# Optimization experiments

Measured on AMD Instinct MI355X. Metric: run time of the kernel, lower is better.

## Reference

```python
import jax, jax.numpy as jnp
import numpy as np

PERIODS = (1, 2, 4, 8)
B, T, D_IN, D_OUT = 64, 2048, 256, 512
N = D_OUT // len(PERIODS)  # 128, per-clock-group width


def setup_inputs() -> dict:
    key = jax.random.key(0)
    ks = jax.random.split(key, 5)
    scale = 1.0 / np.sqrt(N)  # glorot-ish for the (n,n) recurrent mats
    return {
        "X": jax.random.normal(ks[0], (B, T, D_IN), jnp.float32),
        "W": jax.random.uniform(ks[1], (D_IN, D_OUT), jnp.float32, -0.05, 0.05),
        "b": jnp.zeros((D_OUT,), jnp.float32),
        "W_gate": jax.random.uniform(ks[2], (D_IN, D_OUT), jnp.float32, -0.05, 0.05),
        "b_gate": jnp.zeros((D_OUT,), jnp.float32),
        "clock_u": jax.random.normal(ks[3], (len(PERIODS), N, N), jnp.float32) * scale,
        "clock_gates": jax.random.normal(ks[4], (len(PERIODS), N, N), jnp.float32) * scale,
    }


def _hard_sigmoid(x):
    # keras/theano hard_sigmoid: clip(0.2*x + 0.5, 0, 1)
    return jnp.clip(0.2 * x + 0.5, 0.0, 1.0)


def _gating(x_sub, u, u_gate):
    # Faithful to the source: clock_gating passes x_t[:, slice] for ALL THREE of
    # x_t_sub, x_gate_sub, h_tm1_sub (a bug in the original, preserved here).
    k = x_sub @ u                                  # [B, n]
    z = _hard_sigmoid(x_sub + k)                   # update gate (inner_activation)
    q = (x_sub * x_sub) @ u_gate                   # p = x_gate*h_tm1 -> x_sub*x_sub
    z_gate = jnp.tanh(q)                           # gate_activation
    z_out = jax.nn.softplus(x_sub * z_gate)        # activation(s), s = h_tm1*z_gate
    return z * z_out + (1.0 - z) * x_sub           # h_tm1 := x_sub per source bug


def reference(X, W, b, W_gate, b_gate, clock_u, clock_gates):
    # X: [B,T,D_in] -> time-major projections [T,B,D_out]
    x_t = jnp.einsum("bti,io->tbo", X, W) + b
    # x_gate is computed in the source but never consumed due to the slicing
    # bug in clock_gating; DCE'd under jit.
    x_gate = jnp.einsum("bti,io->tbo", X, W_gate) + b_gate  # noqa: F841

    def step(h, inp):
        t, xt = inp
        parts = []
        for i, p in enumerate(PERIODS):
            x_sub = xt[:, i * N:(i + 1) * N]
            new = _gating(x_sub, clock_u[i], clock_gates[i])
            parts.append(jnp.where(t % p == 0, new, h[:, i * N:(i + 1) * N]))
        return jnp.concatenate(parts, axis=1), None

    h0 = jnp.zeros((X.shape[0], D_OUT), X.dtype)
    hT, _ = jax.lax.scan(step, h0, (jnp.arange(x_t.shape[0]), x_t))
    return hT  # return_sequences=False -> last hidden state, [B, D_out]
```

## Files before the change

### kernel.cpp

```cpp
#include <hip/hip_runtime.h>
#include <math.h>


#define TT    2048
#define DIN   256
#define DOUT  512
#define NSUB  128
#define BDIM  64
#define ROWS  8

__global__ __launch_bounds__(256)
void cgrnn_collapsed_kernel(const float* __restrict__ X,
                            const float* __restrict__ W,
                            const float* __restrict__ bias,
                            const float* __restrict__ clock_u,
                            const float* __restrict__ clock_g,
                            float* __restrict__ out)
{
    const int g   = blockIdx.x & 3;
    const int rb  = blockIdx.x >> 2;
    const int r0  = rb * ROWS;
    const int tid = threadIdx.x;
    const int c4  = tid & 31;
    const int r   = tid >> 5;
    const int c   = c4 * 4;

    const int p  = 1 << g;
    const int t  = 2047 - (2047 & (p - 1));

    __shared__ float Xs[ROWS][DIN];
    __shared__ float xs[ROWS][NSUB + 4];

    {
        for (int idx = tid; idx < ROWS * (DIN / 4); idx += 256) {
            const int rr = idx >> 6;
            const int ii = idx & 63;
            const float4 v = *reinterpret_cast<const float4*>(
                X + ((size_t)(r0 + rr) * TT + t) * DIN + ii * 4);
            *reinterpret_cast<float4*>(&Xs[rr][ii * 4]) = v;
        }
    }
    __syncthreads();

    float a0, a1, a2, a3;
    {
        const float* bb = bias + g * NSUB + c;
        a0 = bb[0]; a1 = bb[1]; a2 = bb[2]; a3 = bb[3];
        const float* Wc = W + g * NSUB + c;
#pragma unroll 16
        for (int k = 0; k < DIN; ++k) {
            const float xk = Xs[r][k];
            const float4 wv = *reinterpret_cast<const float4*>(Wc + (size_t)k * DOUT);
            a0 = fmaf(xk, wv.x, a0);
            a1 = fmaf(xk, wv.y, a1);
            a2 = fmaf(xk, wv.z, a2);
            a3 = fmaf(xk, wv.w, a3);
        }
        xs[r][c + 0] = a0;
        xs[r][c + 1] = a1;
        xs[r][c + 2] = a2;
        xs[r][c + 3] = a3;
    }
    __syncthreads();

    float k0 = 0.f, k1 = 0.f, k2 = 0.f, k3 = 0.f;
    float q0 = 0.f, q1 = 0.f, q2 = 0.f, q3 = 0.f;
    {
        const float* ub = clock_u + (size_t)g * NSUB * NSUB + c;
        const float* gb = clock_g + (size_t)g * NSUB * NSUB + c;
#pragma unroll 8
        for (int j = 0; j < NSUB; ++j) {
            const float xv  = xs[r][j];
            const float xv2 = xv * xv;
            const float4 uv = *reinterpret_cast<const float4*>(ub + j * NSUB);
            const float4 gv = *reinterpret_cast<const float4*>(gb + j * NSUB);
            k0 = fmaf(xv, uv.x, k0);  k1 = fmaf(xv, uv.y, k1);
            k2 = fmaf(xv, uv.z, k2);  k3 = fmaf(xv, uv.w, k3);
            q0 = fmaf(xv2, gv.x, q0); q1 = fmaf(xv2, gv.y, q1);
            q2 = fmaf(xv2, gv.z, q2); q3 = fmaf(xv2, gv.w, q3);
        }
    }

    float xr[4] = {a0, a1, a2, a3};
    float kk[4] = {k0, k1, k2, k3};
    float qq[4] = {q0, q1, q2, q3};
    float4 res;
    float* rp = reinterpret_cast<float*>(&res);
#pragma unroll
    for (int i = 0; i < 4; ++i) {
        const float x  = xr[i];
        float z = 0.2f * (x + kk[i]) + 0.5f;
        z = fminf(fmaxf(z, 0.0f), 1.0f);
        const float zg = tanhf(qq[i]);
        const float a  = x * zg;
        const float zo = fmaxf(a, 0.0f) + log1pf(expf(-fabsf(a)));
        rp[i] = z * zo + (1.0f - z) * x;
    }

    *reinterpret_cast<float4*>(out + (size_t)(r0 + r) * DOUT + g * NSUB + c) = res;
}

extern "C" void kernel_launch(void* const* d_in, const int* in_sizes, int n_in,
                              void* d_out, int out_size, void* d_ws, size_t ws_size,
                              hipStream_t stream)
{
    const float* X       = (const float*)d_in[0];
    const float* W       = (const float*)d_in[1];
    const float* bias    = (const float*)d_in[2];
    const float* clock_u = (const float*)d_in[5];
    const float* clock_g = (const float*)d_in[6];
    float* out           = (float*)d_out;

    dim3 grid(4 * (BDIM / ROWS));
    dim3 block(256);
    cgrnn_collapsed_kernel<<<grid, block, 0, stream>>>(X, W, bias, clock_u, clock_g, out);
}
```

Measured before the change: 199.9 us.

## Split reduction across warps and launch one block per batch row and group

Each block now handles one batch row for one clock group instead of eight rows. The input-projection and recurrent-matrix dot products are split across the eight warps along the reduction dimension, then combined through shared-memory partial sums. This raises the grid from 32 to 256 blocks and shortens each thread's serial FMA chain, to fill more compute units and cut latency. In exchange, weights are fetched once per batch row rather than shared across eight rows, and the kernel adds extra barriers and shared-memory traffic.

```diff
diff --git a/kernel.cpp b/kernel.cpp
--- a/kernel.cpp
+++ b/kernel.cpp
@@ -6,8 +6,6 @@
 #define DIN   256
 #define DOUT  512
 #define NSUB  128
-#define BDIM  64
-#define ROWS  8
 
 __global__ __launch_bounds__(256)
 void cgrnn_collapsed_kernel(const float* __restrict__ X,
@@ -18,59 +16,61 @@
                             float* __restrict__ out)
 {
     const int g   = blockIdx.x & 3;
-    const int rb  = blockIdx.x >> 2;
-    const int r0  = rb * ROWS;
+    const int b   = blockIdx.x >> 2;
     const int tid = threadIdx.x;
     const int c4  = tid & 31;
-    const int r   = tid >> 5;
-    const int c   = c4 * 4;
+    const int h   = tid >> 5;
+    const int t   = 2047 - (2047 & ((1 << g) - 1));
 
-    const int p  = 1 << g;
-    const int t  = 2047 - (2047 & (p - 1));
+    __shared__ float Xr[DIN];
+    __shared__ float xs[NSUB];
+    __shared__ float partA[8][NSUB];
+    __shared__ float partK[8][NSUB];
+    __shared__ float partQ[8][NSUB];
 
-    __shared__ float Xs[ROWS][DIN];
-    __shared__ float xs[ROWS][NSUB + 4];
-
-    {
-        for (int idx = tid; idx < ROWS * (DIN / 4); idx += 256) {
-            const int rr = idx >> 6;
-            const int ii = idx & 63;
-            const float4 v = *reinterpret_cast<const float4*>(
-                X + ((size_t)(r0 + rr) * TT + t) * DIN + ii * 4);
-            *reinterpret_cast<float4*>(&Xs[rr][ii * 4]) = v;
-        }
+    if (tid < DIN / 4) {
+        reinterpret_cast<float4*>(Xr)[tid] =
+            reinterpret_cast<const float4*>(X + ((size_t)b * TT + t) * DIN)[tid];
     }
     __syncthreads();
 
-    float a0, a1, a2, a3;
     {
-        const float* bb = bias + g * NSUB + c;
-        a0 = bb[0]; a1 = bb[1]; a2 = bb[2]; a3 = bb[3];
-        const float* Wc = W + g * NSUB + c;
-#pragma unroll 16
-        for (int k = 0; k < DIN; ++k) {
-            const float xk = Xs[r][k];
+        float a0 = 0.f, a1 = 0.f, a2 = 0.f, a3 = 0.f;
+        const float* Wc = W + g * NSUB + c4 * 4;
+#pragma unroll
+        for (int kk = 0; kk < 32; ++kk) {
+            const int k = h * 32 + kk;
+            const float xk = Xr[k];
             const float4 wv = *reinterpret_cast<const float4*>(Wc + (size_t)k * DOUT);
             a0 = fmaf(xk, wv.x, a0);
             a1 = fmaf(xk, wv.y, a1);
             a2 = fmaf(xk, wv.z, a2);
             a3 = fmaf(xk, wv.w, a3);
         }
-        xs[r][c + 0] = a0;
-        xs[r][c + 1] = a1;
-        xs[r][c + 2] = a2;
-        xs[r][c + 3] = a3;
+        partA[h][c4 * 4 + 0] = a0;
+        partA[h][c4 * 4 + 1] = a1;
+        partA[h][c4 * 4 + 2] = a2;
+        partA[h][c4 * 4 + 3] = a3;
     }
     __syncthreads();
 
-    float k0 = 0.f, k1 = 0.f, k2 = 0.f, k3 = 0.f;
-    float q0 = 0.f, q1 = 0.f, q2 = 0.f, q3 = 0.f;
+    if (tid < NSUB) {
+        float s = bias[g * NSUB + tid];
+#pragma unroll
+        for (int hh = 0; hh < 8; ++hh) s += partA[hh][tid];
+        xs[tid] = s;
+    }
+    __syncthreads();
+
     {
-        const float* ub = clock_u + (size_t)g * NSUB * NSUB + c;
-        const float* gb = clock_g + (size_t)g * NSUB * NSUB + c;
-#pragma unroll 8
-        for (int j = 0; j < NSUB; ++j) {
-            const float xv  = xs[r][j];
+        float k0 = 0.f, k1 = 0.f, k2 = 0.f, k3 = 0.f;
+        float q0 = 0.f, q1 = 0.f, q2 = 0.f, q3 = 0.f;
+        const float* ub = clock_u + (size_t)g * NSUB * NSUB + c4 * 4;
+        const float* gb = clock_g + (size_t)g * NSUB * NSUB + c4 * 4;
+#pragma unroll
+        for (int jj = 0; jj < 16; ++jj) {
+            const int j = h * 16 + jj;
+            const float xv  = xs[j];
             const float xv2 = xv * xv;
             const float4 uv = *reinterpret_cast<const float4*>(ub + j * NSUB);
             const float4 gv = *reinterpret_cast<const float4*>(gb + j * NSUB);
@@ -79,25 +79,25 @@
             q0 = fmaf(xv2, gv.x, q0); q1 = fmaf(xv2, gv.y, q1);
             q2 = fmaf(xv2, gv.z, q2); q3 = fmaf(xv2, gv.w, q3);
         }
+        partK[h][c4 * 4 + 0] = k0;  partQ[h][c4 * 4 + 0] = q0;
+        partK[h][c4 * 4 + 1] = k1;  partQ[h][c4 * 4 + 1] = q1;
+        partK[h][c4 * 4 + 2] = k2;  partQ[h][c4 * 4 + 2] = q2;
+        partK[h][c4 * 4 + 3] = k3;  partQ[h][c4 * 4 + 3] = q3;
     }
+    __syncthreads();
 
-    float xr[4] = {a0, a1, a2, a3};
-    float kk[4] = {k0, k1, k2, k3};
-    float qq[4] = {q0, q1, q2, q3};
-    float4 res;
-    float* rp = reinterpret_cast<float*>(&res);
+    if (tid < NSUB) {
+        float ks = 0.f, qs = 0.f;
 #pragma unroll
-    for (int i = 0; i < 4; ++i) {
-        const float x  = xr[i];
-        float z = 0.2f * (x + kk[i]) + 0.5f;
+        for (int hh = 0; hh < 8; ++hh) { ks += partK[hh][tid]; qs += partQ[hh][tid]; }
+        const float x = xs[tid];
+        float z = 0.2f * (x + ks) + 0.5f;
         z = fminf(fmaxf(z, 0.0f), 1.0f);
-        const float zg = tanhf(qq[i]);
+        const float zg = tanhf(qs);
         const float a  = x * zg;
         const float zo = fmaxf(a, 0.0f) + log1pf(expf(-fabsf(a)));
-        rp[i] = z * zo + (1.0f - z) * x;
+        out[(size_t)b * DOUT + g * NSUB + tid] = z * zo + (1.0f - z) * x;
     }
-
-    *reinterpret_cast<float4*>(out + (size_t)(r0 + r) * DOUT + g * NSUB + c) = res;
 }
 
 extern "C" void kernel_launch(void* const* d_in, const int* in_sizes, int n_in,
@@ -111,7 +111,7 @@
     const float* clock_g = (const float*)d_in[6];
     float* out           = (float*)d_out;
 
-    dim3 grid(4 * (BDIM / ROWS));
+    dim3 grid(256);
     dim3 block(256);
     cgrnn_collapsed_kernel<<<grid, block, 0, stream>>>(X, W, bias, clock_u, clock_g, out);
 }
```

Measured after the change: 173.9 us. 1.15x faster.
